# Kernel tuning notes

Measured on AMD Instinct MI355X. Metric: run time of the kernel, lower is better.

Reference implementation:

```python
import jax, jax.numpy as jnp
from jax import lax
import numpy as np

WINDOW = 15  # window_size from init


def setup_inputs() -> dict:
    key = jax.random.key(0)
    img = jax.random.uniform(key, (16, 3, 1024, 1024), dtype=jnp.float32)
    return {"img": img}


def _min_pool2d(x, sz):
    # Separable sliding-window min (erosion with SZxSZ rect kernel),
    # border handled with +inf padding == cv2.erode default border for erosion.
    pad = sz // 2
    inf = jnp.array(jnp.inf, dtype=x.dtype)
    # vertical pass over H
    x = lax.reduce_window(x, inf, lax.min,
                          window_dimensions=(1, 1, sz, 1),
                          window_strides=(1, 1, 1, 1),
                          padding=[(0, 0), (0, 0), (pad, pad), (0, 0)])
    # horizontal pass over W
    x = lax.reduce_window(x, inf, lax.min,
                          window_dimensions=(1, 1, 1, sz),
                          window_strides=(1, 1, 1, 1),
                          padding=[(0, 0), (0, 0), (0, 0), (pad, pad)])
    return x


def reference(img) -> jnp.ndarray:
    # img: [B, C, H, W] -> channel-min -> [B, 1, H, W]
    cmin = jnp.min(img, axis=1, keepdims=True)
    # 15x15 rectangular erosion (min filter), same spatial size
    dark = _min_pool2d(cmin, WINDOW)
    return dark
```

## Files before the change

### kernel.cpp

```cpp
#include <hip/hip_runtime.h>


#define IMG_H 1024
#define IMG_W 1024
#define IMG_C 3
#define IMG_B 16
#define TY    16
#define TX    256
#define HALO  8
#define BW    (TX + 2*HALO)
#define ROWS  (TY + 14)
#define NCH   (BW / 4)
#define NT    256
#define RAD   7

__device__ __forceinline__ float4 min4(float4 a, float4 b) {
    return make_float4(fminf(a.x, b.x), fminf(a.y, b.y),
                       fminf(a.z, b.z), fminf(a.w, b.w));
}

__global__ __launch_bounds__(NT, 4)
void DarkChannel_77713138254515_kernel(const float* __restrict__ img,
                                       float* __restrict__ out) {
    __shared__ float buf[ROWS][BW];

    const int t  = threadIdx.x;
    const int x0 = blockIdx.x * TX;
    const int y0 = blockIdx.y * TY;
    const int b  = blockIdx.z;

    const size_t plane = (size_t)IMG_H * IMG_W;
    const float* imgb = img + (size_t)b * IMG_C * plane;
    float* outb = out + (size_t)b * plane;
    const float INF = __builtin_inff();
    const float4 INF4 = make_float4(INF, INF, INF, INF);

#pragma unroll
    for (int k = 0; k < 8; ++k) {
        int task = t + NT * k;
        if (task < ROWS * NCH) {
            int r  = task / NCH;
            int ch = task - r * NCH;
            int y  = y0 - RAD + r;
            int gx = x0 - HALO + 4 * ch;
            bool ok = ((unsigned)y < IMG_H) & ((unsigned)gx <= IMG_W - 4);
            int yc  = min(max(y, 0), IMG_H - 1);
            int gxc = min(max(gx, 0), IMG_W - 4);
            const float* p0 = imgb + (size_t)yc * IMG_W + gxc;
            float4 v0 = *(const float4*)(p0);
            float4 v1 = *(const float4*)(p0 + plane);
            float4 v2 = *(const float4*)(p0 + 2 * plane);
            float4 v  = min4(v0, min4(v1, v2));
            if (!ok) v = INF4;
            *(float4*)&buf[r][4 * ch] = v;
        }
    }
    __syncthreads();

    for (int c = t; c < BW; c += NT) {
        float col[ROWS];
#pragma unroll
        for (int r = 0; r < ROWS; ++r) col[r] = buf[r][c];
        float S[15];
        S[14] = col[14];
#pragma unroll
        for (int i = 13; i >= 0; --i) S[i] = fminf(col[i], S[i + 1]);
        buf[0][c] = S[0];
        float p = col[15];
#pragma unroll
        for (int i = 1; i < 15; ++i) {
            buf[i][c] = fminf(S[i], p);
            p = fminf(p, col[15 + i]);
        }
        buf[15][c] = p;
    }
    __syncthreads();

#pragma unroll
    for (int k = 0; k < 4; ++k) {
        int task = t + NT * k;
        int r  = task >> 6;
        int ch = task & 63;
        const float* row = &buf[r][4 * ch];
        float2 P[10];
#pragma unroll
        for (int j = 0; j < 10; ++j) P[j] = *(const float2*)(row + 2 * j);
        float2 m2 = P[2];
#pragma unroll
        for (int j = 3; j <= 7; ++j) {
            m2.x = fminf(m2.x, P[j].x); m2.y = fminf(m2.y, P[j].y);
        }
        float core = fminf(m2.x, m2.y);
        float4 o;
        o.x = fminf(core, fminf(P[0].y, fminf(P[1].x, P[1].y)));
        o.y = fminf(core, fminf(P[1].x, fminf(P[1].y, P[8].x)));
        o.z = fminf(core, fminf(P[1].y, fminf(P[8].x, P[8].y)));
        o.w = fminf(core, fminf(P[8].x, fminf(P[8].y, P[9].x)));
        *(float4*)(outb + (size_t)(y0 + r) * IMG_W + x0 + 4 * ch) = o;
    }
}

extern "C" void kernel_launch(void* const* d_in, const int* in_sizes, int n_in,
                              void* d_out, int out_size, void* d_ws, size_t ws_size,
                              hipStream_t stream) {
    const float* img = (const float*)d_in[0];
    float* out = (float*)d_out;

    dim3 grid(IMG_W / TX,
              IMG_H / TY,
              IMG_B);
    DarkChannel_77713138254515_kernel<<<grid, dim3(NT), 0, stream>>>(img, out);
}
```

Before: 298.3 us.

## Double tile height, swizzle 1D grid across XCDs, vectorize horizontal LDS reads

Doubles the rows each block produces from 16 to 32, so the 14-row vertical halo is loaded relative to more output. This cuts the redundant three-channel global reads. The 3D grid becomes a 1D grid of 2048 blocks with a bit swizzle, so vertically adjacent tiles land on the same XCD and can share halo rows in L2. The vertical pass is extended to produce 32 rows from 46 inputs, and the horizontal pass reads shared memory with float4 instead of float2. Occupancy drops to 3 blocks per CU because of the larger LDS tile, and each thread holds more registers.

After: 303.8 us. About the same (+1.9%).

```diff
diff --git a/kernel.cpp b/kernel.cpp
--- a/kernel.cpp
+++ b/kernel.cpp
@@ -5,7 +5,7 @@
 #define IMG_W 1024
 #define IMG_C 3
 #define IMG_B 16
-#define TY    16
+#define TY    32
 #define TX    256
 #define HALO  8
 #define BW    (TX + 2*HALO)
@@ -13,21 +13,25 @@
 #define NCH   (BW / 4)
 #define NT    256
 #define RAD   7
+#define NTASK (ROWS * NCH)
 
 __device__ __forceinline__ float4 min4(float4 a, float4 b) {
     return make_float4(fminf(a.x, b.x), fminf(a.y, b.y),
                        fminf(a.z, b.z), fminf(a.w, b.w));
 }
 
-__global__ __launch_bounds__(NT, 4)
+__global__ __launch_bounds__(NT, 3)
 void DarkChannel_77713138254515_kernel(const float* __restrict__ img,
                                        float* __restrict__ out) {
     __shared__ float buf[ROWS][BW];
 
-    const int t  = threadIdx.x;
-    const int x0 = blockIdx.x * TX;
-    const int y0 = blockIdx.y * TY;
-    const int b  = blockIdx.z;
+    const int t = threadIdx.x;
+
+    const int bid = blockIdx.x;
+    const int swz = ((bid & 7) << 8) | (bid >> 3);
+    const int x0 = (swz & 3) * TX;
+    const int y0 = ((swz >> 2) & 31) * TY;
+    const int b  = swz >> 7;
 
     const size_t plane = (size_t)IMG_H * IMG_W;
     const float* imgb = img + (size_t)b * IMG_C * plane;
@@ -36,9 +40,9 @@
     const float4 INF4 = make_float4(INF, INF, INF, INF);
 
 #pragma unroll
-    for (int k = 0; k < 8; ++k) {
+    for (int k = 0; k < 13; ++k) {
         int task = t + NT * k;
-        if (task < ROWS * NCH) {
+        if (task < NTASK) {
             int r  = task / NCH;
             int ch = task - r * NCH;
             int y  = y0 - RAD + r;
@@ -61,6 +65,7 @@
         float col[ROWS];
 #pragma unroll
         for (int r = 0; r < ROWS; ++r) col[r] = buf[r][c];
+
         float S[15];
         S[14] = col[14];
 #pragma unroll
@@ -72,30 +77,43 @@
             buf[i][c] = fminf(S[i], p);
             p = fminf(p, col[15 + i]);
         }
-        buf[15][c] = p;
+
+        float S1[15];
+        S1[14] = col[29];
+#pragma unroll
+        for (int i = 13; i >= 0; --i) S1[i] = fminf(col[15 + i], S1[i + 1]);
+        buf[15][c] = S1[0];
+        float q = col[30];
+#pragma unroll
+        for (int i = 1; i < 15; ++i) {
+            buf[15 + i][c] = fminf(S1[i], q);
+            q = fminf(q, col[30 + i]);
+        }
+
+        buf[30][c] = q;
+        float s = col[45];
+#pragma unroll
+        for (int i = 44; i >= 31; --i) s = fminf(s, col[i]);
+        buf[31][c] = s;
     }
     __syncthreads();
 
 #pragma unroll
-    for (int k = 0; k < 4; ++k) {
+    for (int k = 0; k < 8; ++k) {
         int task = t + NT * k;
         int r  = task >> 6;
         int ch = task & 63;
         const float* row = &buf[r][4 * ch];
-        float2 P[10];
+        float4 Q[5];
 #pragma unroll
-        for (int j = 0; j < 10; ++j) P[j] = *(const float2*)(row + 2 * j);
-        float2 m2 = P[2];
-#pragma unroll
-        for (int j = 3; j <= 7; ++j) {
-            m2.x = fminf(m2.x, P[j].x); m2.y = fminf(m2.y, P[j].y);
-        }
-        float core = fminf(m2.x, m2.y);
+        for (int j = 0; j < 5; ++j) Q[j] = *(const float4*)(row + 4 * j);
+        float4 m4 = min4(Q[1], min4(Q[2], Q[3]));
+        float core = fminf(fminf(m4.x, m4.y), fminf(m4.z, m4.w));
         float4 o;
-        o.x = fminf(core, fminf(P[0].y, fminf(P[1].x, P[1].y)));
-        o.y = fminf(core, fminf(P[1].x, fminf(P[1].y, P[8].x)));
-        o.z = fminf(core, fminf(P[1].y, fminf(P[8].x, P[8].y)));
-        o.w = fminf(core, fminf(P[8].x, fminf(P[8].y, P[9].x)));
+        o.x = fminf(core, fminf(Q[0].y, fminf(Q[0].z, Q[0].w)));
+        o.y = fminf(core, fminf(Q[0].z, fminf(Q[0].w, Q[4].x)));
+        o.z = fminf(core, fminf(Q[0].w, fminf(Q[4].x, Q[4].y)));
+        o.w = fminf(core, fminf(Q[4].x, fminf(Q[4].y, Q[4].z)));
         *(float4*)(outb + (size_t)(y0 + r) * IMG_W + x0 + 4 * ch) = o;
     }
 }
@@ -106,8 +124,5 @@
     const float* img = (const float*)d_in[0];
     float* out = (float*)d_out;
 
-    dim3 grid(IMG_W / TX,
-              IMG_H / TY,
-              IMG_B);
-    DarkChannel_77713138254515_kernel<<<grid, dim3(NT), 0, stream>>>(img, out);
+    DarkChannel_77713138254515_kernel<<<dim3(2048), dim3(NT), 0, stream>>>(img, out);
 }
```
